# Kernel optimization log

Measured on AMD Instinct MI355X. Metric: run time of the kernel, lower is better.

## Reference

```python
import jax, jax.numpy as jnp
import numpy as np

NEG_SLOPE = 0.2
MASK_FILL = -9e10


def setup_inputs() -> dict:
    key = jax.random.key(0)
    ks = jax.random.split(key, 9)
    B, n_ope, n_mac = 32, 2048, 1024
    total = 64
    ope_dim, mac_dim, out_dim = 64, 64, 128
    ope_ma_adj = jax.random.randint(ks[0], (total, n_ope, n_mac), 0, 2, dtype=jnp.int32)
    batch_idxes = jax.random.randint(ks[1], (B,), 0, total, dtype=jnp.int64)
    feat_ope = jax.random.normal(ks[2], (B, n_ope, ope_dim), dtype=jnp.float32)
    feat_mac = jax.random.normal(ks[3], (B, n_mac, mac_dim), dtype=jnp.float32)
    # parameters (xavier-normal-like scaling)
    def xavier(k, shape):
        fan_in, fan_out = shape[1], shape[0]
        std = jnp.sqrt(2.0 / (fan_in + fan_out))
        return std * jax.random.normal(k, shape, dtype=jnp.float32)
    ope_w = xavier(ks[4], (out_dim, ope_dim))   # Linear weight [out, in]
    mac_w = xavier(ks[5], (out_dim, mac_dim))
    ope_alpha = xavier(ks[6], (out_dim, 1))
    mac_alpha = xavier(ks[7], (out_dim, 1))
    res_w = xavier(ks[8], (out_dim, mac_dim))
    return {
        "ope_ma_adj": ope_ma_adj, "batch_idxes": batch_idxes,
        "feat_ope": feat_ope, "feat_mac": feat_mac,
        "ope_w": ope_w, "mac_w": mac_w,
        "ope_alpha": ope_alpha, "mac_alpha": mac_alpha, "res_w": res_w,
    }


def reference(ope_ma_adj, batch_idxes, feat_ope, feat_mac,
              ope_w, mac_w, ope_alpha, mac_alpha, res_w):
    # dropout p=0 -> identity
    h_ope = jnp.einsum('bod,kd->bok', feat_ope, ope_w)   # [B, n_ope, out]
    h_mac = jnp.einsum('bmd,kd->bmk', feat_mac, mac_w)   # [B, n_mac, out]
    attn_ope = jnp.einsum('bok,k->bo', h_ope, ope_alpha[:, 0])  # [B, n_ope]
    attn_mac = jnp.einsum('bmk,k->bm', h_mac, mac_alpha[:, 0])  # [B, n_mac]
    e = attn_ope[:, :, None] + attn_mac[:, None, :]             # [B, n_ope, n_mac]
    e = jnp.where(e >= 0, e, NEG_SLOPE * e)                      # leaky relu
    mask = ope_ma_adj[batch_idxes] == 1                          # [B, n_ope, n_mac]
    e = jnp.where(mask, e, MASK_FILL)
    alpha = jax.nn.softmax(e, axis=-2)                           # over operations
    out = jnp.einsum('bom,bok->bmk', alpha, h_ope)               # [B, n_mac, out]
    h_res = jnp.einsum('bmd,kd->bmk', feat_mac, res_w)
    return out + h_res
```

## Files before the change

kernel.cpp:

```cpp
#include <hip/hip_runtime.h>

#define N_OPE 2048
#define N_MAC 1024
#define DIM   64
#define KOUT  128
#define NB    32

typedef __attribute__((ext_vector_type(8))) short short8;
typedef __attribute__((ext_vector_type(4))) float floatx4;

static __device__ __forceinline__ unsigned short f2bf(float f) {
    unsigned int u = __builtin_bit_cast(unsigned int, f);
    u += 0x7fffu + ((u >> 16) & 1u);
    return (unsigned short)(u >> 16);
}
static __device__ __forceinline__ float bf2f(unsigned short h) {
    unsigned int u = ((unsigned int)h) << 16;
    return __builtin_bit_cast(float, u);
}

__global__ void k_wa(const float* __restrict__ ow, const float* __restrict__ mw,
                     const float* __restrict__ oa, const float* __restrict__ ma,
                     float* __restrict__ wa)
{
    int t = threadIdx.x;
    const float* w = (t < 64) ? ow : mw;
    const float* a = (t < 64) ? oa : ma;
    int d = t & 63;
    float s = 0.f;
    #pragma unroll 8
    for (int n = 0; n < KOUT; ++n) s = fmaf(w[n * DIM + d], a[n], s);
    wa[t] = s;
}

__global__ __launch_bounds__(256, 2) void k_ope(const float* __restrict__ feat,
        const float* __restrict__ w, const float* __restrict__ wa,
        unsigned short* __restrict__ h_t, float* __restrict__ attn)
{
    int wid = threadIdx.x >> 6, lane = threadIdx.x & 63;
    int L = lane & 15, q = lane >> 4;
    int base = blockIdx.x * 128 + wid * 32;
    int b = base >> 11;
    int o0w = base & (N_OPE - 1);

    float fA[2][2][8];
    #pragma unroll
    for (int mf = 0; mf < 2; ++mf) {
        const float* fr = feat + (size_t)(base + mf * 16 + L) * DIM + q * 8;
        #pragma unroll
        for (int ks = 0; ks < 2; ++ks) {
            float4 v0 = *(const float4*)(fr + ks * 32);
            float4 v1 = *(const float4*)(fr + ks * 32 + 4);
            fA[mf][ks][0] = v0.x; fA[mf][ks][1] = v0.y; fA[mf][ks][2] = v0.z; fA[mf][ks][3] = v0.w;
            fA[mf][ks][4] = v1.x; fA[mf][ks][5] = v1.y; fA[mf][ks][6] = v1.z; fA[mf][ks][7] = v1.w;
        }
    }

    float wav[2][8];
    #pragma unroll
    for (int ks = 0; ks < 2; ++ks) {
        float4 w0 = *(const float4*)(wa + ks * 32 + q * 8);
        float4 w1 = *(const float4*)(wa + ks * 32 + q * 8 + 4);
        wav[ks][0] = w0.x; wav[ks][1] = w0.y; wav[ks][2] = w0.z; wav[ks][3] = w0.w;
        wav[ks][4] = w1.x; wav[ks][5] = w1.y; wav[ks][6] = w1.z; wav[ks][7] = w1.w;
    }
    float part[2] = {0.f, 0.f};
    #pragma unroll
    for (int mf = 0; mf < 2; ++mf)
        #pragma unroll
        for (int ks = 0; ks < 2; ++ks)
            #pragma unroll
            for (int j = 0; j < 8; ++j)
                part[mf] = fmaf(fA[mf][ks][j], wav[ks][j], part[mf]);
    part[0] += __shfl_xor(part[0], 16); part[0] += __shfl_xor(part[0], 32);
    part[1] += __shfl_xor(part[1], 16); part[1] += __shfl_xor(part[1], 32);
    if (q == 0) {
        attn[base + L]      = part[0];
        attn[base + 16 + L] = part[1];
    }

    short8 Ah[2][2], Al[2][2];
    #pragma unroll
    for (int mf = 0; mf < 2; ++mf)
        #pragma unroll
        for (int ks = 0; ks < 2; ++ks)
            #pragma unroll
            for (int j = 0; j < 8; ++j) {
                float x = fA[mf][ks][j];
                unsigned short h = f2bf(x);
                Ah[mf][ks][j] = (short)h;
                Al[mf][ks][j] = (short)f2bf(x - bf2f(h));
            }

    floatx4 C[2][8];
    #pragma unroll
    for (int mf = 0; mf < 2; ++mf)
        #pragma unroll
        for (int nf = 0; nf < 8; ++nf) C[mf][nf] = (floatx4)0.f;

    #pragma unroll
    for (int ks = 0; ks < 2; ++ks) {
        #pragma unroll
        for (int nf = 0; nf < 8; ++nf) {
            const float* wp = w + (size_t)(nf * 16 + L) * DIM + ks * 32 + q * 8;
            float4 u0 = *(const float4*)(wp);
            float4 u1 = *(const float4*)(wp + 4);
            float bw[8] = {u0.x, u0.y, u0.z, u0.w, u1.x, u1.y, u1.z, u1.w};
            short8 Bh, Bl;
            #pragma unroll
            for (int j = 0; j < 8; ++j) {
                unsigned short h = f2bf(bw[j]);
                Bh[j] = (short)h;
                Bl[j] = (short)f2bf(bw[j] - bf2f(h));
            }
            #pragma unroll
            for (int mf = 0; mf < 2; ++mf) {
                C[mf][nf] = __builtin_amdgcn_mfma_f32_16x16x32_bf16(Ah[mf][ks], Bh, C[mf][nf], 0, 0, 0);
                C[mf][nf] = __builtin_amdgcn_mfma_f32_16x16x32_bf16(Al[mf][ks], Bh, C[mf][nf], 0, 0, 0);
                C[mf][nf] = __builtin_amdgcn_mfma_f32_16x16x32_bf16(Ah[mf][ks], Bl, C[mf][nf], 0, 0, 0);
            }
        }
    }

    __shared__ unsigned short T[4][128 * 34];
    #pragma unroll
    for (int mf = 0; mf < 2; ++mf)
        #pragma unroll
        for (int nf = 0; nf < 8; ++nf)
            #pragma unroll
            for (int r = 0; r < 4; ++r)
                T[wid][(nf * 16 + L) * 34 + mf * 16 + q * 4 + r] = f2bf(C[mf][nf][r]);
    __syncthreads();
    unsigned short* htb = h_t + (size_t)b * KOUT * N_OPE;
    #pragma unroll 4
    for (int t = 0; t < 32; ++t) {
        int n = t * 4 + q;
        ushort2 v = *(const ushort2*)&T[wid][n * 34 + 2 * L];
        *(ushort2*)(htb + (size_t)n * N_OPE + o0w + 2 * L) = v;
    }
}

__global__ __launch_bounds__(256, 2) void k_mac(const float* __restrict__ feat,
        const float* __restrict__ w, const float* __restrict__ wa,
        float* __restrict__ h_res, float* __restrict__ attn)
{
    int wid = threadIdx.x >> 6, lane = threadIdx.x & 63;
    int L = lane & 15, q = lane >> 4;
    int base = blockIdx.x * 128 + wid * 32;

    float fA[2][2][8];
    #pragma unroll
    for (int mf = 0; mf < 2; ++mf) {
        const float* fr = feat + (size_t)(base + mf * 16 + L) * DIM + q * 8;
        #pragma unroll
        for (int ks = 0; ks < 2; ++ks) {
            float4 v0 = *(const float4*)(fr + ks * 32);
            float4 v1 = *(const float4*)(fr + ks * 32 + 4);
            fA[mf][ks][0] = v0.x; fA[mf][ks][1] = v0.y; fA[mf][ks][2] = v0.z; fA[mf][ks][3] = v0.w;
            fA[mf][ks][4] = v1.x; fA[mf][ks][5] = v1.y; fA[mf][ks][6] = v1.z; fA[mf][ks][7] = v1.w;
        }
    }

    float wav[2][8];
    #pragma unroll
    for (int ks = 0; ks < 2; ++ks) {
        float4 w0 = *(const float4*)(wa + ks * 32 + q * 8);
        float4 w1 = *(const float4*)(wa + ks * 32 + q * 8 + 4);
        wav[ks][0] = w0.x; wav[ks][1] = w0.y; wav[ks][2] = w0.z; wav[ks][3] = w0.w;
        wav[ks][4] = w1.x; wav[ks][5] = w1.y; wav[ks][6] = w1.z; wav[ks][7] = w1.w;
    }
    float part[2] = {0.f, 0.f};
    #pragma unroll
    for (int mf = 0; mf < 2; ++mf)
        #pragma unroll
        for (int ks = 0; ks < 2; ++ks)
            #pragma unroll
            for (int j = 0; j < 8; ++j)
                part[mf] = fmaf(fA[mf][ks][j], wav[ks][j], part[mf]);
    part[0] += __shfl_xor(part[0], 16); part[0] += __shfl_xor(part[0], 32);
    part[1] += __shfl_xor(part[1], 16); part[1] += __shfl_xor(part[1], 32);
    if (q == 0) {
        attn[base + L]      = part[0];
        attn[base + 16 + L] = part[1];
    }

    short8 Ah[2][2], Al[2][2];
    #pragma unroll
    for (int mf = 0; mf < 2; ++mf)
        #pragma unroll
        for (int ks = 0; ks < 2; ++ks)
            #pragma unroll
            for (int j = 0; j < 8; ++j) {
                float x = fA[mf][ks][j];
                unsigned short h = f2bf(x);
                Ah[mf][ks][j] = (short)h;
                Al[mf][ks][j] = (short)f2bf(x - bf2f(h));
            }

    floatx4 C[2][8];
    #pragma unroll
    for (int mf = 0; mf < 2; ++mf)
        #pragma unroll
        for (int nf = 0; nf < 8; ++nf) C[mf][nf] = (floatx4)0.f;

    #pragma unroll
    for (int ks = 0; ks < 2; ++ks) {
        #pragma unroll
        for (int nf = 0; nf < 8; ++nf) {
            const float* wp = w + (size_t)(nf * 16 + L) * DIM + ks * 32 + q * 8;
            float4 u0 = *(const float4*)(wp);
            float4 u1 = *(const float4*)(wp + 4);
            float bw[8] = {u0.x, u0.y, u0.z, u0.w, u1.x, u1.y, u1.z, u1.w};
            short8 Bh, Bl;
            #pragma unroll
            for (int j = 0; j < 8; ++j) {
                unsigned short h = f2bf(bw[j]);
                Bh[j] = (short)h;
                Bl[j] = (short)f2bf(bw[j] - bf2f(h));
            }
            #pragma unroll
            for (int mf = 0; mf < 2; ++mf) {
                C[mf][nf] = __builtin_amdgcn_mfma_f32_16x16x32_bf16(Ah[mf][ks], Bh, C[mf][nf], 0, 0, 0);
                C[mf][nf] = __builtin_amdgcn_mfma_f32_16x16x32_bf16(Al[mf][ks], Bh, C[mf][nf], 0, 0, 0);
                C[mf][nf] = __builtin_amdgcn_mfma_f32_16x16x32_bf16(Ah[mf][ks], Bl, C[mf][nf], 0, 0, 0);
            }
        }
    }

    #pragma unroll
    for (int mf = 0; mf < 2; ++mf)
        #pragma unroll
        for (int nf = 0; nf < 8; ++nf)
            #pragma unroll
            for (int r = 0; r < 4; ++r)
                h_res[(size_t)(base + mf * 16 + q * 4 + r) * KOUT + nf * 16 + L] = C[mf][nf][r];
}

__global__ __launch_bounds__(128) void k_attn(const int* __restrict__ adj,
        const int* __restrict__ bidx,
        const unsigned short* __restrict__ h_t,
        const float* __restrict__ attn_ope, const float* __restrict__ attn_mac,
        const float* __restrict__ h_res, float* __restrict__ out)
{
    int b  = blockIdx.y;
    int m0 = blockIdx.x * 32;
    int wv = threadIdx.x >> 6;
    int lane = threadIdx.x & 63;
    int L = lane & 15, q = lane >> 4;
    const int* adjt = adj + (size_t)bidx[b] * N_OPE * N_MAC;
    const unsigned short* htb = h_t + (size_t)b * KOUT * N_OPE;
    const float* aob = attn_ope + b * N_OPE;
    float am0 = attn_mac[b * N_MAC + m0 + L];
    float am1 = attn_mac[b * N_MAC + m0 + 16 + L];

    floatx4 C0[8], C1[8];
    #pragma unroll
    for (int i = 0; i < 8; ++i) { C0[i] = (floatx4)0.f; C1[i] = (floatx4)0.f; }
    float den0 = 0.f, den1 = 0.f;

    int oBeg = wv * (N_OPE / 2), oEnd = oBeg + (N_OPE / 2);
    for (int o0 = oBeg; o0 < oEnd; o0 += 32) {
        int ob = o0 + q * 8;
        float4 aoA = *(const float4*)(aob + ob);
        float4 aoB = *(const float4*)(aob + ob + 4);
        float ao[8] = {aoA.x, aoA.y, aoA.z, aoA.w, aoB.x, aoB.y, aoB.z, aoB.w};

        short8 Bf[8];
        #pragma unroll
        for (int nf = 0; nf < 8; ++nf)
            Bf[nf] = *(const short8*)(htb + (size_t)(nf * 16 + L) * N_OPE + ob);

        int mk0[8], mk1[8];
        #pragma unroll
        for (int j = 0; j < 8; ++j) {
            mk0[j] = adjt[(size_t)(ob + j) * N_MAC + m0 + L];
            mk1[j] = adjt[(size_t)(ob + j) * N_MAC + m0 + 16 + L];
        }

        short8 A0, A1;
        #pragma unroll
        for (int j = 0; j < 8; ++j) {
            float e0 = ao[j] + am0;
            e0 = fmaxf(e0, 0.2f * e0);
            float w0 = (mk0[j] == 1) ? __expf(e0) : 0.f;
            den0 += w0;
            A0[j] = (short)f2bf(w0);
            float e1 = ao[j] + am1;
            e1 = fmaxf(e1, 0.2f * e1);
            float w1 = (mk1[j] == 1) ? __expf(e1) : 0.f;
            den1 += w1;
            A1[j] = (short)f2bf(w1);
        }

        #pragma unroll
        for (int nf = 0; nf < 8; ++nf) {
            C0[nf] = __builtin_amdgcn_mfma_f32_16x16x32_bf16(A0, Bf[nf], C0[nf], 0, 0, 0);
            C1[nf] = __builtin_amdgcn_mfma_f32_16x16x32_bf16(A1, Bf[nf], C1[nf], 0, 0, 0);
        }
    }

    den0 += __shfl_xor(den0, 16); den0 += __shfl_xor(den0, 32);
    den1 += __shfl_xor(den1, 16); den1 += __shfl_xor(den1, 32);

    __shared__ float CS[32 * 132];
    __shared__ float DS[2][32];
    if (wv == 1) {
        #pragma unroll
        for (int fm = 0; fm < 2; ++fm) {
            const floatx4* Cf = fm ? C1 : C0;
            #pragma unroll
            for (int nf = 0; nf < 8; ++nf)
                #pragma unroll
                for (int r = 0; r < 4; ++r)
                    CS[(fm * 16 + q * 4 + r) * 132 + nf * 16 + L] = Cf[nf][r];
        }
        if (q == 0) { DS[1][L] = den0; DS[1][16 + L] = den1; }
    } else {
        if (q == 0) { DS[0][L] = den0; DS[0][16 + L] = den1; }
    }
    __syncthreads();

    if (wv == 0) {
        #pragma unroll
        for (int fm = 0; fm < 2; ++fm) {
            const floatx4* Cf = fm ? C1 : C0;
            #pragma unroll
            for (int r = 0; r < 4; ++r) {
                int m = fm * 16 + q * 4 + r;
                float inv = 1.0f / (DS[0][m] + DS[1][m]);
                size_t obase = ((size_t)b * N_MAC + m0 + m) * KOUT;
                #pragma unroll
                for (int nf = 0; nf < 8; ++nf) {
                    int n = nf * 16 + L;
                    float v = Cf[nf][r] + CS[m * 132 + n];
                    out[obase + n] = v * inv + h_res[obase + n];
                }
            }
        }
    }
}

extern "C" void kernel_launch(void* const* d_in, const int* in_sizes, int n_in,
                              void* d_out, int out_size, void* d_ws, size_t ws_size,
                              hipStream_t stream) {
    const int*   adj       = (const int*)d_in[0];
    const int*   bidx      = (const int*)d_in[1];
    const float* feat_ope  = (const float*)d_in[2];
    const float* feat_mac  = (const float*)d_in[3];
    const float* ope_w     = (const float*)d_in[4];
    const float* mac_w     = (const float*)d_in[5];
    const float* ope_alpha = (const float*)d_in[6];
    const float* mac_alpha = (const float*)d_in[7];
    const float* res_w     = (const float*)d_in[8];
    float* out = (float*)d_out;

    char* ws = (char*)d_ws;
    unsigned short* h_t = (unsigned short*)ws;
    float* attn_ope = (float*)(ws + (size_t)(16 << 20));
    float* attn_mac = (float*)(ws + (size_t)(16 << 20) + (256 << 10));
    float* wa       = (float*)(ws + (size_t)(16 << 20) + (384 << 10));
    float* h_res    = (float*)(ws + (size_t)(17 << 20));

    k_wa<<<1, 128, 0, stream>>>(ope_w, mac_w, ope_alpha, mac_alpha, wa);
    k_ope<<<512, 256, 0, stream>>>(feat_ope, ope_w, wa, h_t, attn_ope);
    k_mac<<<256, 256, 0, stream>>>(feat_mac, res_w, wa + 64, h_res, attn_mac);
    k_attn<<<dim3(N_MAC / 32, NB), 128, 0, stream>>>(adj, bidx, h_t, attn_ope,
                                                     attn_mac, h_res, out);
}
```

Measured before the change: 733.4 us.

## Fuse mac projection into attention kernel and factor exp of leaky-relu scores

Removes the separate weight-alpha and mac kernels. The mac attention scores and the residual projection are now computed inside the attention kernel, so h_res is no longer written to and read back from global memory. The ope kernel now derives its attention score from the MFMA accumulators and stores exp(s) and exp(0.2 s), which turns the per-element exp in the attention loop into products and a select. The attention kernel also goes from 2 to 4 waves per block, each covering a quarter of the operations, with an LDS reduction at the end. The factored exp can overflow or lose precision for large scores, and the resulting softmax is not max-stabilised.

Result: faster. 718.5 us (-2.0%).

```diff
diff --git a/kernel.cpp b/kernel.cpp
--- a/kernel.cpp
+++ b/kernel.cpp
@@ -19,23 +19,9 @@
     return __builtin_bit_cast(float, u);
 }
 
-__global__ void k_wa(const float* __restrict__ ow, const float* __restrict__ mw,
-                     const float* __restrict__ oa, const float* __restrict__ ma,
-                     float* __restrict__ wa)
-{
-    int t = threadIdx.x;
-    const float* w = (t < 64) ? ow : mw;
-    const float* a = (t < 64) ? oa : ma;
-    int d = t & 63;
-    float s = 0.f;
-    #pragma unroll 8
-    for (int n = 0; n < KOUT; ++n) s = fmaf(w[n * DIM + d], a[n], s);
-    wa[t] = s;
-}
-
 __global__ __launch_bounds__(256, 2) void k_ope(const float* __restrict__ feat,
-        const float* __restrict__ w, const float* __restrict__ wa,
-        unsigned short* __restrict__ h_t, float* __restrict__ attn)
+        const float* __restrict__ w, const float* __restrict__ alpha,
+        unsigned short* __restrict__ h_t, float2* __restrict__ pq)
 {
     int wid = threadIdx.x >> 6, lane = threadIdx.x & 63;
     int L = lane & 15, q = lane >> 4;
@@ -56,29 +42,6 @@
         }
     }
 
-    float wav[2][8];
-    #pragma unroll
-    for (int ks = 0; ks < 2; ++ks) {
-        float4 w0 = *(const float4*)(wa + ks * 32 + q * 8);
-        float4 w1 = *(const float4*)(wa + ks * 32 + q * 8 + 4);
-        wav[ks][0] = w0.x; wav[ks][1] = w0.y; wav[ks][2] = w0.z; wav[ks][3] = w0.w;
-        wav[ks][4] = w1.x; wav[ks][5] = w1.y; wav[ks][6] = w1.z; wav[ks][7] = w1.w;
-    }
-    float part[2] = {0.f, 0.f};
-    #pragma unroll
-    for (int mf = 0; mf < 2; ++mf)
-        #pragma unroll
-        for (int ks = 0; ks < 2; ++ks)
-            #pragma unroll
-            for (int j = 0; j < 8; ++j)
-                part[mf] = fmaf(fA[mf][ks][j], wav[ks][j], part[mf]);
-    part[0] += __shfl_xor(part[0], 16); part[0] += __shfl_xor(part[0], 32);
-    part[1] += __shfl_xor(part[1], 16); part[1] += __shfl_xor(part[1], 32);
-    if (q == 0) {
-        attn[base + L]      = part[0];
-        attn[base + 16 + L] = part[1];
-    }
-
     short8 Ah[2][2], Al[2][2];
     #pragma unroll
     for (int mf = 0; mf < 2; ++mf)
@@ -122,6 +85,23 @@
         }
     }
 
+    float alf[8];
+    #pragma unroll
+    for (int nf = 0; nf < 8; ++nf) alf[nf] = alpha[nf * 16 + L];
+    #pragma unroll
+    for (int mf = 0; mf < 2; ++mf) {
+        #pragma unroll
+        for (int r = 0; r < 4; ++r) {
+            float s = 0.f;
+            #pragma unroll
+            for (int nf = 0; nf < 8; ++nf) s = fmaf(C[mf][nf][r], alf[nf], s);
+            s += __shfl_xor(s, 1); s += __shfl_xor(s, 2);
+            s += __shfl_xor(s, 4); s += __shfl_xor(s, 8);
+            if (L == 0)
+                pq[base + mf * 16 + q * 4 + r] = make_float2(__expf(s), __expf(0.2f * s));
+        }
+    }
+
     __shared__ unsigned short T[4][128 * 34];
     #pragma unroll
     for (int mf = 0; mf < 2; ++mf)
@@ -140,18 +120,158 @@
     }
 }
 
-__global__ __launch_bounds__(256, 2) void k_mac(const float* __restrict__ feat,
-        const float* __restrict__ w, const float* __restrict__ wa,
-        float* __restrict__ h_res, float* __restrict__ attn)
+__global__ __launch_bounds__(256, 3) void k_attn(const int* __restrict__ adj,
+        const int* __restrict__ bidx,
+        const unsigned short* __restrict__ h_t,
+        const float2* __restrict__ pq,
+        const float* __restrict__ feat_mac,
+        const float* __restrict__ mac_w, const float* __restrict__ mac_alpha,
+        const float* __restrict__ res_w,
+        float* __restrict__ out)
 {
-    int wid = threadIdx.x >> 6, lane = threadIdx.x & 63;
+    int b  = blockIdx.y;
+    int m0 = blockIdx.x * 32;
+    int t  = threadIdx.x;
+    int wv = t >> 6;
+    int lane = t & 63;
     int L = lane & 15, q = lane >> 4;
-    int base = blockIdx.x * 128 + wid * 32;
+
+    __shared__ float buf0[32 * 132];
+    __shared__ float buf1[32 * 132];
+    __shared__ float waS[64];
+    __shared__ float amS[32];
+    __shared__ float DS[4][32];
+
+    {
+        int d = t & 63, seg = t >> 6;
+        float p = 0.f;
+        #pragma unroll 8
+        for (int n = seg * 32; n < seg * 32 + 32; ++n)
+            p = fmaf(mac_w[n * DIM + d], mac_alpha[n], p);
+        buf0[seg * 64 + d] = p;
+    }
+    __syncthreads();
+    if (t < 64) waS[t] = buf0[t] + buf0[64 + t] + buf0[128 + t] + buf0[192 + t];
+    __syncthreads();
+    {
+        int row = t & 31, seg = t >> 5;
+        const float* fr = feat_mac + ((size_t)b * N_MAC + m0 + row) * DIM + seg * 8;
+        float p = 0.f;
+        #pragma unroll
+        for (int k = 0; k < 8; ++k) p = fmaf(fr[k], waS[seg * 8 + k], p);
+        buf1[seg * 32 + row] = p;
+    }
+    __syncthreads();
+    if (t < 32) {
+        float s = 0.f;
+        #pragma unroll
+        for (int sg = 0; sg < 8; ++sg) s += buf1[sg * 32 + t];
+        amS[t] = s;
+    }
+    __syncthreads();
+
+    float am0 = amS[L], am1 = amS[16 + L];
+    float pM0 = __expf(am0), qM0 = __expf(0.2f * am0);
+    float pM1 = __expf(am1), qM1 = __expf(0.2f * am1);
+
+    const int* adjt = adj + (size_t)bidx[b] * N_OPE * N_MAC;
+    const unsigned short* htb = h_t + (size_t)b * KOUT * N_OPE;
+    const float2* pqb = pq + (size_t)b * N_OPE;
+
+    floatx4 C0[8], C1[8];
+    #pragma unroll
+    for (int i = 0; i < 8; ++i) { C0[i] = (floatx4)0.f; C1[i] = (floatx4)0.f; }
+    float den0 = 0.f, den1 = 0.f;
+
+    int oBeg = wv * (N_OPE / 4);
+    for (int o0 = oBeg; o0 < oBeg + N_OPE / 4; o0 += 32) {
+        int ob = o0 + q * 8;
+        float4 pv0 = *(const float4*)(pqb + ob);
+        float4 pv1 = *(const float4*)(pqb + ob + 2);
+        float4 pv2 = *(const float4*)(pqb + ob + 4);
+        float4 pv3 = *(const float4*)(pqb + ob + 6);
+        float pA[8] = {pv0.x, pv0.z, pv1.x, pv1.z, pv2.x, pv2.z, pv3.x, pv3.z};
+        float qA[8] = {pv0.y, pv0.w, pv1.y, pv1.w, pv2.y, pv2.w, pv3.y, pv3.w};
+
+        short8 Bf[8];
+        #pragma unroll
+        for (int nf = 0; nf < 8; ++nf)
+            Bf[nf] = *(const short8*)(htb + (size_t)(nf * 16 + L) * N_OPE + ob);
+
+        int mk0[8], mk1[8];
+        #pragma unroll
+        for (int j = 0; j < 8; ++j) {
+            mk0[j] = adjt[(size_t)(ob + j) * N_MAC + m0 + L];
+            mk1[j] = adjt[(size_t)(ob + j) * N_MAC + m0 + 16 + L];
+        }
+
+        float w0v[8], w1v[8];
+        #pragma unroll
+        for (int j = 0; j < 8; ++j) {
+            float tp0 = pA[j] * pM0;
+            float w0 = (tp0 >= 1.0f) ? tp0 : qA[j] * qM0;
+            w0 = (mk0[j] == 1) ? w0 : 0.f;
+            den0 += w0; w0v[j] = w0;
+            float tp1 = pA[j] * pM1;
+            float w1 = (tp1 >= 1.0f) ? tp1 : qA[j] * qM1;
+            w1 = (mk1[j] == 1) ? w1 : 0.f;
+            den1 += w1; w1v[j] = w1;
+        }
+        int4 A0i, A1i;
+        #pragma unroll
+        for (int j2 = 0; j2 < 4; ++j2) {
+            unsigned lo0 = __builtin_bit_cast(unsigned, w0v[2 * j2])     + 0x8000u;
+            unsigned hi0 = __builtin_bit_cast(unsigned, w0v[2 * j2 + 1]) + 0x8000u;
+            ((unsigned*)&A0i)[j2] = __builtin_amdgcn_perm(hi0, lo0, 0x07060302u);
+            unsigned lo1 = __builtin_bit_cast(unsigned, w1v[2 * j2])     + 0x8000u;
+            unsigned hi1 = __builtin_bit_cast(unsigned, w1v[2 * j2 + 1]) + 0x8000u;
+            ((unsigned*)&A1i)[j2] = __builtin_amdgcn_perm(hi1, lo1, 0x07060302u);
+        }
+        short8 A0 = __builtin_bit_cast(short8, A0i);
+        short8 A1 = __builtin_bit_cast(short8, A1i);
+
+        #pragma unroll
+        for (int nf = 0; nf < 8; ++nf) {
+            C0[nf] = __builtin_amdgcn_mfma_f32_16x16x32_bf16(A0, Bf[nf], C0[nf], 0, 0, 0);
+            C1[nf] = __builtin_amdgcn_mfma_f32_16x16x32_bf16(A1, Bf[nf], C1[nf], 0, 0, 0);
+        }
+    }
+
+    den0 += __shfl_xor(den0, 16); den0 += __shfl_xor(den0, 32);
+    den1 += __shfl_xor(den1, 16); den1 += __shfl_xor(den1, 32);
+    if (q == 0) { DS[wv][L] = den0; DS[wv][16 + L] = den1; }
+
+    if (wv == 0 || wv == 2) {
+        float* bp = (wv == 0) ? buf0 : buf1;
+        #pragma unroll
+        for (int mf = 0; mf < 2; ++mf) {
+            const floatx4* Cf = mf ? C1 : C0;
+            #pragma unroll
+            for (int nf = 0; nf < 8; ++nf)
+                #pragma unroll
+                for (int r = 0; r < 4; ++r)
+                    bp[(mf * 16 + q * 4 + r) * 132 + nf * 16 + L] = Cf[nf][r];
+        }
+    }
+    __syncthreads();
+    if (wv == 1 || wv == 3) {
+        float* bp = (wv == 1) ? buf0 : buf1;
+        #pragma unroll
+        for (int mf = 0; mf < 2; ++mf) {
+            const floatx4* Cf = mf ? C1 : C0;
+            #pragma unroll
+            for (int nf = 0; nf < 8; ++nf)
+                #pragma unroll
+                for (int r = 0; r < 4; ++r)
+                    bp[(mf * 16 + q * 4 + r) * 132 + nf * 16 + L] += Cf[nf][r];
+        }
+    }
+    __syncthreads();
 
     float fA[2][2][8];
     #pragma unroll
     for (int mf = 0; mf < 2; ++mf) {
-        const float* fr = feat + (size_t)(base + mf * 16 + L) * DIM + q * 8;
+        const float* fr = feat_mac + ((size_t)b * N_MAC + m0 + mf * 16 + L) * DIM + q * 8;
         #pragma unroll
         for (int ks = 0; ks < 2; ++ks) {
             float4 v0 = *(const float4*)(fr + ks * 32);
@@ -160,30 +280,6 @@
             fA[mf][ks][4] = v1.x; fA[mf][ks][5] = v1.y; fA[mf][ks][6] = v1.z; fA[mf][ks][7] = v1.w;
         }
     }
-
-    float wav[2][8];
-    #pragma unroll
-    for (int ks = 0; ks < 2; ++ks) {
-        float4 w0 = *(const float4*)(wa + ks * 32 + q * 8);
-        float4 w1 = *(const float4*)(wa + ks * 32 + q * 8 + 4);
-        wav[ks][0] = w0.x; wav[ks][1] = w0.y; wav[ks][2] = w0.z; wav[ks][3] = w0.w;
-        wav[ks][4] = w1.x; wav[ks][5] = w1.y; wav[ks][6] = w1.z; wav[ks][7] = w1.w;
-    }
-    float part[2] = {0.f, 0.f};
-    #pragma unroll
-    for (int mf = 0; mf < 2; ++mf)
-        #pragma unroll
-        for (int ks = 0; ks < 2; ++ks)
-            #pragma unroll
-            for (int j = 0; j < 8; ++j)
-                part[mf] = fmaf(fA[mf][ks][j], wav[ks][j], part[mf]);
-    part[0] += __shfl_xor(part[0], 16); part[0] += __shfl_xor(part[0], 32);
-    part[1] += __shfl_xor(part[1], 16); part[1] += __shfl_xor(part[1], 32);
-    if (q == 0) {
-        attn[base + L]      = part[0];
-        attn[base + 16 + L] = part[1];
-    }
-
     short8 Ah[2][2], Al[2][2];
     #pragma unroll
     for (int mf = 0; mf < 2; ++mf)
@@ -196,18 +292,14 @@
                 Ah[mf][ks][j] = (short)h;
                 Al[mf][ks][j] = (short)f2bf(x - bf2f(h));
             }
-
-    floatx4 C[2][8];
-    #pragma unroll
-    for (int mf = 0; mf < 2; ++mf)
-        #pragma unroll
-        for (int nf = 0; nf < 8; ++nf) C[mf][nf] = (floatx4)0.f;
-
+    floatx4 R[2][2];
+    R[0][0] = (floatx4)0.f; R[0][1] = (floatx4)0.f;
+    R[1][0] = (floatx4)0.f; R[1][1] = (floatx4)0.f;
     #pragma unroll
     for (int ks = 0; ks < 2; ++ks) {
         #pragma unroll
-        for (int nf = 0; nf < 8; ++nf) {
-            const float* wp = w + (size_t)(nf * 16 + L) * DIM + ks * 32 + q * 8;
+        for (int nfl = 0; nfl < 2; ++nfl) {
+            const float* wp = res_w + (size_t)((wv * 2 + nfl) * 16 + L) * DIM + ks * 32 + q * 8;
             float4 u0 = *(const float4*)(wp);
             float4 u1 = *(const float4*)(wp + 4);
             float bw[8] = {u0.x, u0.y, u0.z, u0.w, u1.x, u1.y, u1.z, u1.w};
@@ -220,121 +312,25 @@
             }
             #pragma unroll
             for (int mf = 0; mf < 2; ++mf) {
-                C[mf][nf] = __builtin_amdgcn_mfma_f32_16x16x32_bf16(Ah[mf][ks], Bh, C[mf][nf], 0, 0, 0);
-                C[mf][nf] = __builtin_amdgcn_mfma_f32_16x16x32_bf16(Al[mf][ks], Bh, C[mf][nf], 0, 0, 0);
-                C[mf][nf] = __builtin_amdgcn_mfma_f32_16x16x32_bf16(Ah[mf][ks], Bl, C[mf][nf], 0, 0, 0);
-            }
-        }
-    }
-
-    #pragma unroll
-    for (int mf = 0; mf < 2; ++mf)
-        #pragma unroll
-        for (int nf = 0; nf < 8; ++nf)
-            #pragma unroll
-            for (int r = 0; r < 4; ++r)
-                h_res[(size_t)(base + mf * 16 + q * 4 + r) * KOUT + nf * 16 + L] = C[mf][nf][r];
-}
-
-__global__ __launch_bounds__(128) void k_attn(const int* __restrict__ adj,
-        const int* __restrict__ bidx,
-        const unsigned short* __restrict__ h_t,
-        const float* __restrict__ attn_ope, const float* __restrict__ attn_mac,
-        const float* __restrict__ h_res, float* __restrict__ out)
-{
-    int b  = blockIdx.y;
-    int m0 = blockIdx.x * 32;
-    int wv = threadIdx.x >> 6;
-    int lane = threadIdx.x & 63;
-    int L = lane & 15, q = lane >> 4;
-    const int* adjt = adj + (size_t)bidx[b] * N_OPE * N_MAC;
-    const unsigned short* htb = h_t + (size_t)b * KOUT * N_OPE;
-    const float* aob = attn_ope + b * N_OPE;
-    float am0 = attn_mac[b * N_MAC + m0 + L];
-    float am1 = attn_mac[b * N_MAC + m0 + 16 + L];
-
-    floatx4 C0[8], C1[8];
-    #pragma unroll
-    for (int i = 0; i < 8; ++i) { C0[i] = (floatx4)0.f; C1[i] = (floatx4)0.f; }
-    float den0 = 0.f, den1 = 0.f;
-
-    int oBeg = wv * (N_OPE / 2), oEnd = oBeg + (N_OPE / 2);
-    for (int o0 = oBeg; o0 < oEnd; o0 += 32) {
-        int ob = o0 + q * 8;
-        float4 aoA = *(const float4*)(aob + ob);
-        float4 aoB = *(const float4*)(aob + ob + 4);
-        float ao[8] = {aoA.x, aoA.y, aoA.z, aoA.w, aoB.x, aoB.y, aoB.z, aoB.w};
-
-        short8 Bf[8];
-        #pragma unroll
-        for (int nf = 0; nf < 8; ++nf)
-            Bf[nf] = *(const short8*)(htb + (size_t)(nf * 16 + L) * N_OPE + ob);
-
-        int mk0[8], mk1[8];
-        #pragma unroll
-        for (int j = 0; j < 8; ++j) {
-            mk0[j] = adjt[(size_t)(ob + j) * N_MAC + m0 + L];
-            mk1[j] = adjt[(size_t)(ob + j) * N_MAC + m0 + 16 + L];
-        }
-
-        short8 A0, A1;
-        #pragma unroll
-        for (int j = 0; j < 8; ++j) {
-            float e0 = ao[j] + am0;
-            e0 = fmaxf(e0, 0.2f * e0);
-            float w0 = (mk0[j] == 1) ? __expf(e0) : 0.f;
-            den0 += w0;
-            A0[j] = (short)f2bf(w0);
-            float e1 = ao[j] + am1;
-            e1 = fmaxf(e1, 0.2f * e1);
-            float w1 = (mk1[j] == 1) ? __expf(e1) : 0.f;
-            den1 += w1;
-            A1[j] = (short)f2bf(w1);
-        }
-
-        #pragma unroll
-        for (int nf = 0; nf < 8; ++nf) {
-            C0[nf] = __builtin_amdgcn_mfma_f32_16x16x32_bf16(A0, Bf[nf], C0[nf], 0, 0, 0);
-            C1[nf] = __builtin_amdgcn_mfma_f32_16x16x32_bf16(A1, Bf[nf], C1[nf], 0, 0, 0);
-        }
-    }
-
-    den0 += __shfl_xor(den0, 16); den0 += __shfl_xor(den0, 32);
-    den1 += __shfl_xor(den1, 16); den1 += __shfl_xor(den1, 32);
-
-    __shared__ float CS[32 * 132];
-    __shared__ float DS[2][32];
-    if (wv == 1) {
-        #pragma unroll
-        for (int fm = 0; fm < 2; ++fm) {
-            const floatx4* Cf = fm ? C1 : C0;
-            #pragma unroll
-            for (int nf = 0; nf < 8; ++nf)
-                #pragma unroll
-                for (int r = 0; r < 4; ++r)
-                    CS[(fm * 16 + q * 4 + r) * 132 + nf * 16 + L] = Cf[nf][r];
-        }
-        if (q == 0) { DS[1][L] = den0; DS[1][16 + L] = den1; }
-    } else {
-        if (q == 0) { DS[0][L] = den0; DS[0][16 + L] = den1; }
-    }
-    __syncthreads();
-
-    if (wv == 0) {
-        #pragma unroll
-        for (int fm = 0; fm < 2; ++fm) {
-            const floatx4* Cf = fm ? C1 : C0;
-            #pragma unroll
-            for (int r = 0; r < 4; ++r) {
-                int m = fm * 16 + q * 4 + r;
-                float inv = 1.0f / (DS[0][m] + DS[1][m]);
-                size_t obase = ((size_t)b * N_MAC + m0 + m) * KOUT;
-                #pragma unroll
-                for (int nf = 0; nf < 8; ++nf) {
-                    int n = nf * 16 + L;
-                    float v = Cf[nf][r] + CS[m * 132 + n];
-                    out[obase + n] = v * inv + h_res[obase + n];
-                }
+                R[mf][nfl] = __builtin_amdgcn_mfma_f32_16x16x32_bf16(Ah[mf][ks], Bh, R[mf][nfl], 0, 0, 0);
+                R[mf][nfl] = __builtin_amdgcn_mfma_f32_16x16x32_bf16(Al[mf][ks], Bh, R[mf][nfl], 0, 0, 0);
+                R[mf][nfl] = __builtin_amdgcn_mfma_f32_16x16x32_bf16(Ah[mf][ks], Bl, R[mf][nfl], 0, 0, 0);
+            }
+        }
+    }
+
+    #pragma unroll
+    for (int mf = 0; mf < 2; ++mf) {
+        #pragma unroll
+        for (int r = 0; r < 4; ++r) {
+            int row = mf * 16 + q * 4 + r;
+            float inv = 1.0f / (DS[0][row] + DS[1][row] + DS[2][row] + DS[3][row]);
+            size_t obase = ((size_t)b * N_MAC + m0 + row) * KOUT;
+            #pragma unroll
+            for (int nfl = 0; nfl < 2; ++nfl) {
+                int col = (wv * 2 + nfl) * 16 + L;
+                out[obase + col] = (buf0[row * 132 + col] + buf1[row * 132 + col]) * inv
+                                   + R[mf][nfl][r];
             }
         }
     }
@@ -356,14 +352,9 @@
 
     char* ws = (char*)d_ws;
     unsigned short* h_t = (unsigned short*)ws;
-    float* attn_ope = (float*)(ws + (size_t)(16 << 20));
-    float* attn_mac = (float*)(ws + (size_t)(16 << 20) + (256 << 10));
-    float* wa       = (float*)(ws + (size_t)(16 << 20) + (384 << 10));
-    float* h_res    = (float*)(ws + (size_t)(17 << 20));
-
-    k_wa<<<1, 128, 0, stream>>>(ope_w, mac_w, ope_alpha, mac_alpha, wa);
-    k_ope<<<512, 256, 0, stream>>>(feat_ope, ope_w, wa, h_t, attn_ope);
-    k_mac<<<256, 256, 0, stream>>>(feat_mac, res_w, wa + 64, h_res, attn_mac);
-    k_attn<<<dim3(N_MAC / 32, NB), 128, 0, stream>>>(adj, bidx, h_t, attn_ope,
-                                                     attn_mac, h_res, out);
-}
+    float2* pq          = (float2*)(ws + (size_t)(16 << 20));
+
+    k_ope<<<512, 256, 0, stream>>>(feat_ope, ope_w, ope_alpha, h_t, pq);
+    k_attn<<<dim3(N_MAC / 32, NB), 256, 0, stream>>>(adj, bidx, h_t, pq, feat_mac,
+                                                     mac_w, mac_alpha, res_w, out);
+}
```
